# Performance work log

Hardware: AMD Instinct MI355X
Metric: run time of the kernel (lower is better)

Reference implementation:

```python
import jax, jax.numpy as jnp
import numpy as np

B, NN, K, F = 256, 90, 10, 90  # graphs, nodes/graph, retain_node, node_len
TENDENCY = 0.7


def setup_inputs() -> dict:
    key = jax.random.key(0)
    ks = jax.random.split(key, 16)
    N = B * NN
    # fully-connected (no self-loop) edge list per graph, block-offset per graph
    a = np.repeat(np.arange(NN), NN)
    b = np.tile(np.arange(NN), NN)
    m = a != b
    src0, dst0 = a[m], b[m]                      # [8010]
    off = (np.arange(B) * NN)[:, None]
    src = (src0[None, :] + off).ravel()
    dst = (dst0[None, :] + off).ravel()
    edge_index = jnp.asarray(np.stack([src, dst]), dtype=jnp.int64)
    E = edge_index.shape[1]
    batch = jnp.asarray(np.repeat(np.arange(B), NN), dtype=jnp.int64)
    s = 1.0 / np.sqrt(F)
    return {
        "x": jax.random.normal(ks[0], (N, F), jnp.float32),
        "edge_index": edge_index,
        "edge_attr": jax.random.uniform(ks[1], (E,), jnp.float32),
        "batch": batch,
        "W1r": jax.random.normal(ks[2], (F, F), jnp.float32) * s,
        "W1m": jax.random.normal(ks[3], (F, F), jnp.float32) * s,
        "b1": jnp.zeros((F,), jnp.float32),
        "W2r": jax.random.normal(ks[4], (F, F), jnp.float32) * s,
        "W2m": jax.random.normal(ks[5], (F, F), jnp.float32) * s,
        "b2": jnp.zeros((F,), jnp.float32),
        "pool_p": jax.random.normal(ks[6], (F,), jnp.float32),
        "lin_W": jax.random.normal(ks[7], (K * F, 2 * K * F + 1), jnp.float32) / np.sqrt(K * F),
        "lin_b": jnp.zeros((2 * K * F + 1,), jnp.float32),
        "cls_W": jax.random.normal(ks[8], (2 * K * F + 1, 1), jnp.float32) / np.sqrt(2 * K * F + 1),
        "cls_b": jnp.zeros((1,), jnp.float32),
    }


def reference(x, edge_index, edge_attr, batch, W1r, W1m, b1, W2r, W2m, b2,
              pool_p, lin_W, lin_b, cls_W, cls_b):
    src, dst = edge_index[0], edge_index[1]
    N = x.shape[0]

    def conv(h, Wr, Wm, b):  # edge-conditioned message passing
        msg = (h[src] @ Wm) * edge_attr[:, None]          # [E, F]
        agg = jax.ops.segment_sum(msg, dst, num_segments=N)
        return jax.nn.relu(h @ Wr + agg + b)

    def bn(h):  # fresh BatchNorm1d (gamma=1, beta=0), training-mode batch stats
        mu = h.mean(axis=0)
        var = h.var(axis=0)
        return (h - mu) * jax.lax.rsqrt(var + 1e-5)

    x = bn(conv(x, W1r, W1m, b1))
    x = bn(conv(x, W2r, W2m, b2))

    # category-aware top-k pooling: projection score, keep K nodes per graph
    score = TENDENCY * jnp.tanh((x @ pool_p) / jnp.linalg.norm(pool_p))  # [N]
    vals, idx = jax.lax.top_k(score.reshape(B, NN), K)                   # [B, K]
    xb = x.reshape(B, NN, F)
    xs = jnp.take_along_axis(xb, idx[:, :, None], axis=1) * vals[:, :, None]
    perm = (idx + (jnp.arange(B) * NN)[:, None]).reshape(-1)             # global node ids

    h = xs.reshape(B, K * F)
    h = h @ lin_W + lin_b
    out = jax.nn.sigmoid((h @ cls_W + cls_b).reshape(-1))                # [B]
    return (out, perm)
```

## Files before the change

kernel.cpp:

```cpp
#include <hip/hip_runtime.h>
#include <math.h>

#define NG   90
#define PD   96
#define STRD 100
#define KK   10
#define NB   256
#define NTOT (NB*NG)
#define EPG  8010
#define SM_FLOATS (4*PD*STRD + 4*96)

__global__ __launch_bounds__(256)
void prep_v_kernel(const float* __restrict__ linW, const float* __restrict__ linb,
                   const float* __restrict__ clsW, const float* __restrict__ clsb,
                   const float* __restrict__ poolp,
                   float* __restrict__ vlin, float* __restrict__ scal) {
    int b = blockIdx.x, tid = threadIdx.x;
    int lane = tid & 63, w = tid >> 6;
    if (b < 225) {
        int j = b * 4 + w;
        const float* row = linW + (size_t)j * 1801;
        float acc = 0.f;
        for (int c = lane; c < 1801; c += 64) acc += row[c] * clsW[c];
        for (int off = 32; off; off >>= 1) acc += __shfl_down(acc, off);
        if (lane == 0) vlin[j] = acc;
    } else {
        if (w == 0) {
            float acc = 0.f;
            for (int c = lane; c < 1801; c += 64) acc += linb[c] * clsW[c];
            for (int off = 32; off; off >>= 1) acc += __shfl_down(acc, off);
            if (lane == 0) scal[0] = acc + clsb[0];
        } else if (w == 1) {
            float acc = 0.f;
            for (int c = lane; c < NG; c += 64) acc += poolp[c] * poolp[c];
            for (int off = 32; off; off >>= 1) acc += __shfl_down(acc, off);
            if (lane == 0) scal[1] = rsqrtf(acc);
        }
    }
}

__global__ __launch_bounds__(1024, 4)
void layer_kernel(const float* __restrict__ xin, const float* __restrict__ gsIn, int apply_bn,
                  const float* __restrict__ attr,
                  const float* __restrict__ Wm, const float* __restrict__ Wr,
                  const float* __restrict__ bias,
                  float* __restrict__ hout, float* __restrict__ gsOut)
{
    extern __shared__ float sm[];
    float* sX   = sm;
    float* sA   = sX + PD * STRD;
    float* sM   = sA + PD * STRD;
    float* sW   = sM + PD * STRD;
    float* sSum = sW + PD * STRD;
    float* sSq  = sSum + 96;
    float* sMu  = sSq + 96;
    float* sRs  = sMu + 96;

    const int g = blockIdx.x, tid = threadIdx.x;
    const int lane = tid & 63, wave = tid >> 6;
    const int wr = wave >> 2, wc = wave & 3;
    const int lr = lane >> 3, lc = lane & 7;
    const int r0 = (wr * 8 + lr) * 3, c0 = (wc * 8 + lc) * 3;

    if (tid < 96) {
        sSum[tid] = 0.f; sSq[tid] = 0.f;
        float m = 0.f, r = 1.f;
        if (apply_bn && tid < NG) {
            m = gsIn[tid] * (1.f / NTOT);
            float v = gsIn[96 + tid] * (1.f / NTOT) - m * m;
            r = rsqrtf(v + 1e-5f);
        }
        sMu[tid] = m; sRs[tid] = r;
    }
    __syncthreads();

    for (int idx = tid; idx < PD * PD; idx += 1024) {
        int r = idx / PD, k = idx - (idx / PD) * PD;
        float v = 0.f;
        if (r < NG && k < NG) v = (xin[(g * NG + r) * NG + k] - sMu[k]) * sRs[k];
        sX[r * STRD + k] = v;
    }
    for (int idx = tid; idx < PD * PD; idx += 1024) {
        int s = idx / PD, d = idx - (idx / PD) * PD;
        float v = 0.f;
        if (s < NG && d < NG && d != s) v = attr[g * EPG + s * 89 + (d > s ? d - 1 : d)];
        sA[d * STRD + s] = v;
    }
    for (int idx = tid; idx < PD * PD; idx += 1024) {
        int k = idx / PD, c = idx - (idx / PD) * PD;
        float v = (k < NG && c < NG) ? Wm[k * NG + c] : 0.f;
        sW[c * STRD + k] = v;
    }
    float wrg[9];
#pragma unroll
    for (int t = 0; t < 9; t++) {
        int idx = tid + t * 1024;
        int k = idx / PD, c = idx - (idx / PD) * PD;
        wrg[t] = (k < NG && c < NG) ? Wr[k * NG + c] : 0.f;
    }
    float bj[3];
#pragma unroll
    for (int j = 0; j < 3; j++) bj[j] = (c0 + j < NG) ? bias[c0 + j] : 0.f;
    __syncthreads();

    float accM[3][3] = {{0.f,0.f,0.f},{0.f,0.f,0.f},{0.f,0.f,0.f}};
    {
        const float* pX = sX + r0 * STRD;
        const float* pW = sW + c0 * STRD;
#pragma unroll 3
        for (int k = 0; k < PD; k += 4) {
            float4 xv[3], wv[3];
#pragma unroll
            for (int i = 0; i < 3; i++) xv[i] = *(const float4*)(pX + i * STRD + k);
#pragma unroll
            for (int j = 0; j < 3; j++) wv[j] = *(const float4*)(pW + j * STRD + k);
#pragma unroll
            for (int i = 0; i < 3; i++)
#pragma unroll
                for (int j = 0; j < 3; j++) {
                    accM[i][j] = fmaf(xv[i].x, wv[j].x, accM[i][j]);
                    accM[i][j] = fmaf(xv[i].y, wv[j].y, accM[i][j]);
                    accM[i][j] = fmaf(xv[i].z, wv[j].z, accM[i][j]);
                    accM[i][j] = fmaf(xv[i].w, wv[j].w, accM[i][j]);
                }
        }
    }
#pragma unroll
    for (int j = 0; j < 3; j++)
#pragma unroll
        for (int i = 0; i < 3; i++)
            sM[(c0 + j) * STRD + (r0 + i)] = accM[i][j];
    __syncthreads();

#pragma unroll
    for (int t = 0; t < 9; t++) {
        int idx = tid + t * 1024;
        int k = idx / PD, c = idx - (idx / PD) * PD;
        sW[c * STRD + k] = wrg[t];
    }
    __syncthreads();

    float h[3][3];
#pragma unroll
    for (int j = 0; j < 3; j++)
#pragma unroll
        for (int i = 0; i < 3; i++) h[i][j] = bj[j];
    {
        const float* pX = sX + r0 * STRD;
        const float* pA = sA + r0 * STRD;
        const float* pW = sW + c0 * STRD;
        const float* pM = sM + c0 * STRD;
#pragma unroll 2
        for (int k = 0; k < PD; k += 4) {
            float4 xv[3], av[3], wv[3], mv[3];
#pragma unroll
            for (int i = 0; i < 3; i++) {
                xv[i] = *(const float4*)(pX + i * STRD + k);
                av[i] = *(const float4*)(pA + i * STRD + k);
            }
#pragma unroll
            for (int j = 0; j < 3; j++) {
                wv[j] = *(const float4*)(pW + j * STRD + k);
                mv[j] = *(const float4*)(pM + j * STRD + k);
            }
#pragma unroll
            for (int i = 0; i < 3; i++)
#pragma unroll
                for (int j = 0; j < 3; j++) {
                    h[i][j] = fmaf(xv[i].x, wv[j].x, h[i][j]);
                    h[i][j] = fmaf(xv[i].y, wv[j].y, h[i][j]);
                    h[i][j] = fmaf(xv[i].z, wv[j].z, h[i][j]);
                    h[i][j] = fmaf(xv[i].w, wv[j].w, h[i][j]);
                    h[i][j] = fmaf(av[i].x, mv[j].x, h[i][j]);
                    h[i][j] = fmaf(av[i].y, mv[j].y, h[i][j]);
                    h[i][j] = fmaf(av[i].z, mv[j].z, h[i][j]);
                    h[i][j] = fmaf(av[i].w, mv[j].w, h[i][j]);
                }
        }
    }

    float cs[3] = {0.f,0.f,0.f}, cq[3] = {0.f,0.f,0.f};
#pragma unroll
    for (int i = 0; i < 3; i++) {
        int r = r0 + i;
        if (r < NG) {
#pragma unroll
            for (int j = 0; j < 3; j++) {
                int c = c0 + j;
                float v = fmaxf(h[i][j], 0.f);
                if (c < NG) {
                    hout[(size_t)(g * NG + r) * NG + c] = v;
                    cs[j] += v; cq[j] += v * v;
                }
            }
        }
    }
#pragma unroll
    for (int m = 8; m < 64; m <<= 1) {
#pragma unroll
        for (int j = 0; j < 3; j++) {
            cs[j] += __shfl_xor(cs[j], m);
            cq[j] += __shfl_xor(cq[j], m);
        }
    }
    if (lr == 0) {
#pragma unroll
        for (int j = 0; j < 3; j++) {
            int c = c0 + j;
            if (c < NG) { atomicAdd(&sSum[c], cs[j]); atomicAdd(&sSq[c], cq[j]); }
        }
    }
    __syncthreads();
    if (tid < NG) { atomicAdd(&gsOut[tid], sSum[tid]); atomicAdd(&gsOut[96 + tid], sSq[tid]); }
}

__global__ __launch_bounds__(256)
void final_kernel(const float* __restrict__ h2,
                  const float* __restrict__ gsum, const float* __restrict__ gsq,
                  const float* __restrict__ poolp,
                  const float* __restrict__ vlin, const float* __restrict__ scal,
                  float* __restrict__ out)
{
    __shared__ float sXN[NG * 91];
    __shared__ float sMu[96], sRs[96], sP[96];
    __shared__ float sScore[NG];
    __shared__ int   sIdx[KK];
    __shared__ float sVal[KK];
    __shared__ float sRed[4];
    const int g = blockIdx.x, tid = threadIdx.x;

    if (tid < NG) {
        float m = gsum[tid] * (1.f / NTOT);
        float v = gsq[tid] * (1.f / NTOT) - m * m;
        sMu[tid] = m; sRs[tid] = rsqrtf(v + 1e-5f);
        sP[tid] = poolp[tid];
    }
    __syncthreads();

    const float* hg = h2 + (size_t)g * (NG * NG);
    for (int idx = tid; idx < NG * NG; idx += 256) {
        int d = idx / NG, f = idx - (idx / NG) * NG;
        sXN[d * 91 + f] = (hg[idx] - sMu[f]) * sRs[f];
    }
    __syncthreads();

    if (tid < NG) {
        float s = 0.f;
        for (int f = 0; f < NG; f++) s += sXN[tid * 91 + f] * sP[f];
        sScore[tid] = 0.7f * tanhf(s * scal[1]);
    }
    __syncthreads();

    if (tid < 64) {
        float va = sScore[tid];
        float vb = (tid + 64 < NG) ? sScore[tid + 64] : -1e30f;
        int ia = tid, ib = tid + 64;
        for (int k = 0; k < KK; k++) {
            float v; int i;
            if (va >= vb) { v = va; i = ia; } else { v = vb; i = ib; }
            for (int off = 1; off < 64; off <<= 1) {
                float v2 = __shfl_xor(v, off);
                int   i2 = __shfl_xor(i, off);
                if (v2 > v || (v2 == v && i2 < i)) { v = v2; i = i2; }
            }
            if (tid == 0) { sIdx[k] = i; sVal[k] = v; }
            if (i == ia) va = -1e30f;
            if (i == ib) vb = -1e30f;
        }
    }
    __syncthreads();

    if (tid < KK) out[NB + g * KK + tid] = (float)(g * NG + sIdx[tid]);

    float acc = 0.f;
    for (int j = tid; j < KK * NG; j += 256) {
        int k = j / NG, f = j - (j / NG) * NG;
        acc += sXN[sIdx[k] * 91 + f] * sVal[k] * vlin[j];
    }
    for (int off = 32; off; off >>= 1) acc += __shfl_down(acc, off);
    if ((tid & 63) == 0) sRed[tid >> 6] = acc;
    __syncthreads();
    if (tid == 0) {
        float tot = sRed[0] + sRed[1] + sRed[2] + sRed[3] + scal[0];
        out[g] = 1.f / (1.f + expf(-tot));
    }
}

extern "C" void kernel_launch(void* const* d_in, const int* in_sizes, int n_in,
                              void* d_out, int out_size, void* d_ws, size_t ws_size,
                              hipStream_t stream) {
    const float* x    = (const float*)d_in[0];
    const float* attr = (const float*)d_in[2];
    const float* W1r  = (const float*)d_in[4];
    const float* W1m  = (const float*)d_in[5];
    const float* b1   = (const float*)d_in[6];
    const float* W2r  = (const float*)d_in[7];
    const float* W2m  = (const float*)d_in[8];
    const float* b2   = (const float*)d_in[9];
    const float* poolp= (const float*)d_in[10];
    const float* linW = (const float*)d_in[11];
    const float* linb = (const float*)d_in[12];
    const float* clsW = (const float*)d_in[13];
    const float* clsb = (const float*)d_in[14];

    float* ws     = (float*)d_ws;
    float* gstats = ws;
    float* vlin   = ws + 384;
    float* scal   = ws + 1284;
    float* h1     = ws + 2048;
    float* h2     = h1 + (size_t)NTOT * NG;

    hipMemsetAsync(gstats, 0, 384 * sizeof(float), stream);
    prep_v_kernel<<<226, 256, 0, stream>>>(linW, linb, clsW, clsb, poolp, vlin, scal);

    const size_t smem = SM_FLOATS * sizeof(float);
    layer_kernel<<<NB, 1024, smem, stream>>>(x,  gstats, 0, attr, W1m, W1r, b1, h1, gstats);
    layer_kernel<<<NB, 1024, smem, stream>>>(h1, gstats, 1, attr, W2m, W2r, b2, h2, gstats + 192);

    final_kernel<<<NB, 256, 0, stream>>>(h2, gstats + 192, gstats + 288, poolp, vlin, scal, (float*)d_out);
}
```

Measured before the change: 197.1 us.

## Use 6x6 register tiles with 256 threads and fuse prep into layer kernel

Result: slower. 241.7 us (+22.6%).

```diff
diff --git a/kernel.cpp b/kernel.cpp
--- a/kernel.cpp
+++ b/kernel.cpp
@@ -8,59 +8,36 @@
 #define NB   256
 #define NTOT (NB*NG)
 #define EPG  8010
-#define SM_FLOATS (4*PD*STRD + 4*96)
-
-__global__ __launch_bounds__(256)
-void prep_v_kernel(const float* __restrict__ linW, const float* __restrict__ linb,
-                   const float* __restrict__ clsW, const float* __restrict__ clsb,
-                   const float* __restrict__ poolp,
-                   float* __restrict__ vlin, float* __restrict__ scal) {
-    int b = blockIdx.x, tid = threadIdx.x;
-    int lane = tid & 63, w = tid >> 6;
-    if (b < 225) {
-        int j = b * 4 + w;
-        const float* row = linW + (size_t)j * 1801;
-        float acc = 0.f;
-        for (int c = lane; c < 1801; c += 64) acc += row[c] * clsW[c];
-        for (int off = 32; off; off >>= 1) acc += __shfl_down(acc, off);
-        if (lane == 0) vlin[j] = acc;
-    } else {
-        if (w == 0) {
-            float acc = 0.f;
-            for (int c = lane; c < 1801; c += 64) acc += linb[c] * clsW[c];
-            for (int off = 32; off; off >>= 1) acc += __shfl_down(acc, off);
-            if (lane == 0) scal[0] = acc + clsb[0];
-        } else if (w == 1) {
-            float acc = 0.f;
-            for (int c = lane; c < NG; c += 64) acc += poolp[c] * poolp[c];
-            for (int off = 32; off; off >>= 1) acc += __shfl_down(acc, off);
-            if (lane == 0) scal[1] = rsqrtf(acc);
-        }
-    }
-}
-
-__global__ __launch_bounds__(1024, 4)
+#define ARR  (PD*STRD)
+#define SM_FLOATS (4*ARR + 4*96)
+
+__global__ __launch_bounds__(256, 1)
 void layer_kernel(const float* __restrict__ xin, const float* __restrict__ gsIn, int apply_bn,
                   const float* __restrict__ attr,
                   const float* __restrict__ Wm, const float* __restrict__ Wr,
                   const float* __restrict__ bias,
-                  float* __restrict__ hout, float* __restrict__ gsOut)
+                  float* __restrict__ hout, float* __restrict__ gsOut,
+                  int do_prep,
+                  const float* __restrict__ linW, const float* __restrict__ linb,
+                  const float* __restrict__ clsW, const float* __restrict__ clsb,
+                  const float* __restrict__ poolp,
+                  float* __restrict__ vlin, float* __restrict__ scal)
 {
     extern __shared__ float sm[];
-    float* sX   = sm;
-    float* sA   = sX + PD * STRD;
-    float* sM   = sA + PD * STRD;
-    float* sW   = sM + PD * STRD;
-    float* sSum = sW + PD * STRD;
+    float* sXM = sm;
+    float* sA  = sXM + ARR;
+    float* sWm = sA + ARR;
+    float* sWr = sWm + ARR;
+    float* sSum = sWr + ARR;
     float* sSq  = sSum + 96;
     float* sMu  = sSq + 96;
     float* sRs  = sMu + 96;
 
     const int g = blockIdx.x, tid = threadIdx.x;
     const int lane = tid & 63, wave = tid >> 6;
-    const int wr = wave >> 2, wc = wave & 3;
     const int lr = lane >> 3, lc = lane & 7;
-    const int r0 = (wr * 8 + lr) * 3, c0 = (wc * 8 + lc) * 3;
+    const int r0 = (wave >> 1) * 48 + lr * 6;
+    const int c0 = (wave & 1) * 48 + lc * 6;
 
     if (tid < 96) {
         sSum[tid] = 0.f; sSq[tid] = 0.f;
@@ -74,103 +51,92 @@
     }
     __syncthreads();
 
-    for (int idx = tid; idx < PD * PD; idx += 1024) {
+    for (int idx = tid; idx < PD * PD; idx += 256) {
         int r = idx / PD, k = idx - (idx / PD) * PD;
         float v = 0.f;
-        if (r < NG && k < NG) v = (xin[(g * NG + r) * NG + k] - sMu[k]) * sRs[k];
-        sX[r * STRD + k] = v;
-    }
-    for (int idx = tid; idx < PD * PD; idx += 1024) {
-        int s = idx / PD, d = idx - (idx / PD) * PD;
+        if (r < NG && k < NG) v = (xin[(size_t)(g * NG + r) * NG + k] - sMu[k]) * sRs[k];
+        sXM[r * STRD + k] = v;
+    }
+    for (int idx = tid; idx < PD * PD; idx += 256) {
+        int d = idx / PD, s = idx - (idx / PD) * PD;
         float v = 0.f;
-        if (s < NG && d < NG && d != s) v = attr[g * EPG + s * 89 + (d > s ? d - 1 : d)];
+        if (d < NG && s < NG && s != d) v = attr[(size_t)g * EPG + s * 89 + (d > s ? d - 1 : d)];
         sA[d * STRD + s] = v;
     }
-    for (int idx = tid; idx < PD * PD; idx += 1024) {
-        int k = idx / PD, c = idx - (idx / PD) * PD;
-        float v = (k < NG && c < NG) ? Wm[k * NG + c] : 0.f;
-        sW[c * STRD + k] = v;
-    }
-    float wrg[9];
-#pragma unroll
-    for (int t = 0; t < 9; t++) {
-        int idx = tid + t * 1024;
-        int k = idx / PD, c = idx - (idx / PD) * PD;
-        wrg[t] = (k < NG && c < NG) ? Wr[k * NG + c] : 0.f;
-    }
-    float bj[3];
-#pragma unroll
-    for (int j = 0; j < 3; j++) bj[j] = (c0 + j < NG) ? bias[c0 + j] : 0.f;
-    __syncthreads();
-
-    float accM[3][3] = {{0.f,0.f,0.f},{0.f,0.f,0.f},{0.f,0.f,0.f}};
+    for (int idx = tid; idx < PD * PD; idx += 256) {
+        int c = idx / PD, k = idx - (idx / PD) * PD;
+        float vm = 0.f, vr = 0.f;
+        if (c < NG && k < NG) { vm = Wm[k * NG + c]; vr = Wr[k * NG + c]; }
+        sWm[c * STRD + k] = vm;
+        sWr[c * STRD + k] = vr;
+    }
+    float bj[6];
+#pragma unroll
+    for (int j = 0; j < 6; j++) bj[j] = (c0 + j < NG) ? bias[c0 + j] : 0.f;
+    __syncthreads();
+
+    float accM[6][6], accR[6][6];
+#pragma unroll
+    for (int i = 0; i < 6; i++)
+#pragma unroll
+        for (int j = 0; j < 6; j++) { accM[i][j] = 0.f; accR[i][j] = 0.f; }
     {
-        const float* pX = sX + r0 * STRD;
-        const float* pW = sW + c0 * STRD;
-#pragma unroll 3
-        for (int k = 0; k < PD; k += 4) {
-            float4 xv[3], wv[3];
-#pragma unroll
-            for (int i = 0; i < 3; i++) xv[i] = *(const float4*)(pX + i * STRD + k);
-#pragma unroll
-            for (int j = 0; j < 3; j++) wv[j] = *(const float4*)(pW + j * STRD + k);
-#pragma unroll
-            for (int i = 0; i < 3; i++)
-#pragma unroll
-                for (int j = 0; j < 3; j++) {
-                    accM[i][j] = fmaf(xv[i].x, wv[j].x, accM[i][j]);
-                    accM[i][j] = fmaf(xv[i].y, wv[j].y, accM[i][j]);
-                    accM[i][j] = fmaf(xv[i].z, wv[j].z, accM[i][j]);
-                    accM[i][j] = fmaf(xv[i].w, wv[j].w, accM[i][j]);
-                }
-        }
-    }
-#pragma unroll
-    for (int j = 0; j < 3; j++)
-#pragma unroll
-        for (int i = 0; i < 3; i++)
-            sM[(c0 + j) * STRD + (r0 + i)] = accM[i][j];
-    __syncthreads();
-
-#pragma unroll
-    for (int t = 0; t < 9; t++) {
-        int idx = tid + t * 1024;
-        int k = idx / PD, c = idx - (idx / PD) * PD;
-        sW[c * STRD + k] = wrg[t];
-    }
-    __syncthreads();
-
-    float h[3][3];
-#pragma unroll
-    for (int j = 0; j < 3; j++)
-#pragma unroll
-        for (int i = 0; i < 3; i++) h[i][j] = bj[j];
-    {
-        const float* pX = sX + r0 * STRD;
-        const float* pA = sA + r0 * STRD;
-        const float* pW = sW + c0 * STRD;
-        const float* pM = sM + c0 * STRD;
+        const float* pX  = sXM + r0 * STRD;
+        const float* pWm = sWm + c0 * STRD;
+        const float* pWr = sWr + c0 * STRD;
 #pragma unroll 2
         for (int k = 0; k < PD; k += 4) {
-            float4 xv[3], av[3], wv[3], mv[3];
-#pragma unroll
-            for (int i = 0; i < 3; i++) {
-                xv[i] = *(const float4*)(pX + i * STRD + k);
-                av[i] = *(const float4*)(pA + i * STRD + k);
+            float4 xv[6], wm[6], wr[6];
+#pragma unroll
+            for (int i = 0; i < 6; i++) xv[i] = *(const float4*)(pX + i * STRD + k);
+#pragma unroll
+            for (int j = 0; j < 6; j++) {
+                wm[j] = *(const float4*)(pWm + j * STRD + k);
+                wr[j] = *(const float4*)(pWr + j * STRD + k);
             }
 #pragma unroll
-            for (int j = 0; j < 3; j++) {
-                wv[j] = *(const float4*)(pW + j * STRD + k);
-                mv[j] = *(const float4*)(pM + j * STRD + k);
-            }
-#pragma unroll
-            for (int i = 0; i < 3; i++)
-#pragma unroll
-                for (int j = 0; j < 3; j++) {
-                    h[i][j] = fmaf(xv[i].x, wv[j].x, h[i][j]);
-                    h[i][j] = fmaf(xv[i].y, wv[j].y, h[i][j]);
-                    h[i][j] = fmaf(xv[i].z, wv[j].z, h[i][j]);
-                    h[i][j] = fmaf(xv[i].w, wv[j].w, h[i][j]);
+            for (int i = 0; i < 6; i++)
+#pragma unroll
+                for (int j = 0; j < 6; j++) {
+                    accM[i][j] = fmaf(xv[i].x, wm[j].x, accM[i][j]);
+                    accM[i][j] = fmaf(xv[i].y, wm[j].y, accM[i][j]);
+                    accM[i][j] = fmaf(xv[i].z, wm[j].z, accM[i][j]);
+                    accM[i][j] = fmaf(xv[i].w, wm[j].w, accM[i][j]);
+                    accR[i][j] = fmaf(xv[i].x, wr[j].x, accR[i][j]);
+                    accR[i][j] = fmaf(xv[i].y, wr[j].y, accR[i][j]);
+                    accR[i][j] = fmaf(xv[i].z, wr[j].z, accR[i][j]);
+                    accR[i][j] = fmaf(xv[i].w, wr[j].w, accR[i][j]);
+                }
+        }
+    }
+    __syncthreads();
+
+#pragma unroll
+    for (int j = 0; j < 6; j++)
+#pragma unroll
+        for (int i = 0; i < 6; i++)
+            sXM[(c0 + j) * STRD + (r0 + i)] = accM[i][j];
+    __syncthreads();
+
+    float h[6][6];
+#pragma unroll
+    for (int i = 0; i < 6; i++)
+#pragma unroll
+        for (int j = 0; j < 6; j++) h[i][j] = accR[i][j] + bj[j];
+    {
+        const float* pA = sA  + r0 * STRD;
+        const float* pM = sXM + c0 * STRD;
+#pragma unroll 2
+        for (int k = 0; k < PD; k += 4) {
+            float4 av[6], mv[6];
+#pragma unroll
+            for (int i = 0; i < 6; i++) av[i] = *(const float4*)(pA + i * STRD + k);
+#pragma unroll
+            for (int j = 0; j < 6; j++) mv[j] = *(const float4*)(pM + j * STRD + k);
+#pragma unroll
+            for (int i = 0; i < 6; i++)
+#pragma unroll
+                for (int j = 0; j < 6; j++) {
                     h[i][j] = fmaf(av[i].x, mv[j].x, h[i][j]);
                     h[i][j] = fmaf(av[i].y, mv[j].y, h[i][j]);
                     h[i][j] = fmaf(av[i].z, mv[j].z, h[i][j]);
@@ -179,16 +145,18 @@
         }
     }
 
-    float cs[3] = {0.f,0.f,0.f}, cq[3] = {0.f,0.f,0.f};
-#pragma unroll
-    for (int i = 0; i < 3; i++) {
+    float cs[6], cq[6];
+#pragma unroll
+    for (int j = 0; j < 6; j++) { cs[j] = 0.f; cq[j] = 0.f; }
+#pragma unroll
+    for (int i = 0; i < 6; i++) {
         int r = r0 + i;
         if (r < NG) {
 #pragma unroll
-            for (int j = 0; j < 3; j++) {
+            for (int j = 0; j < 6; j++) {
                 int c = c0 + j;
-                float v = fmaxf(h[i][j], 0.f);
                 if (c < NG) {
+                    float v = fmaxf(h[i][j], 0.f);
                     hout[(size_t)(g * NG + r) * NG + c] = v;
                     cs[j] += v; cq[j] += v * v;
                 }
@@ -198,20 +166,43 @@
 #pragma unroll
     for (int m = 8; m < 64; m <<= 1) {
 #pragma unroll
-        for (int j = 0; j < 3; j++) {
+        for (int j = 0; j < 6; j++) {
             cs[j] += __shfl_xor(cs[j], m);
             cq[j] += __shfl_xor(cq[j], m);
         }
     }
     if (lr == 0) {
 #pragma unroll
-        for (int j = 0; j < 3; j++) {
+        for (int j = 0; j < 6; j++) {
             int c = c0 + j;
             if (c < NG) { atomicAdd(&sSum[c], cs[j]); atomicAdd(&sSq[c], cq[j]); }
         }
     }
     __syncthreads();
     if (tid < NG) { atomicAdd(&gsOut[tid], sSum[tid]); atomicAdd(&gsOut[96 + tid], sSq[tid]); }
+
+    if (do_prep) {
+        if (g < 225) {
+            int j = g * 4 + wave;
+            const float* row = linW + (size_t)j * 1801;
+            float acc = 0.f;
+            for (int c = lane; c < 1801; c += 64) acc += row[c] * clsW[c];
+            for (int off = 32; off; off >>= 1) acc += __shfl_down(acc, off);
+            if (lane == 0) vlin[j] = acc;
+        } else if (g == 255) {
+            if (wave == 0) {
+                float acc = 0.f;
+                for (int c = lane; c < 1801; c += 64) acc += linb[c] * clsW[c];
+                for (int off = 32; off; off >>= 1) acc += __shfl_down(acc, off);
+                if (lane == 0) scal[0] = acc + clsb[0];
+            } else if (wave == 1) {
+                float acc = 0.f;
+                for (int c = lane; c < NG; c += 64) acc += poolp[c] * poolp[c];
+                for (int off = 32; off; off >>= 1) acc += __shfl_down(acc, off);
+                if (lane == 0) scal[1] = rsqrtf(acc);
+            }
+        }
+    }
 }
 
 __global__ __launch_bounds__(256)
@@ -311,11 +302,14 @@
     float* h2     = h1 + (size_t)NTOT * NG;
 
     hipMemsetAsync(gstats, 0, 384 * sizeof(float), stream);
-    prep_v_kernel<<<226, 256, 0, stream>>>(linW, linb, clsW, clsb, poolp, vlin, scal);
 
     const size_t smem = SM_FLOATS * sizeof(float);
-    layer_kernel<<<NB, 1024, smem, stream>>>(x,  gstats, 0, attr, W1m, W1r, b1, h1, gstats);
-    layer_kernel<<<NB, 1024, smem, stream>>>(h1, gstats, 1, attr, W2m, W2r, b2, h2, gstats + 192);
+    hipFuncSetAttribute((const void*)layer_kernel, hipFuncAttributeMaxDynamicSharedMemorySize, (int)smem);
+
+    layer_kernel<<<NB, 256, smem, stream>>>(x,  gstats, 0, attr, W1m, W1r, b1, h1, gstats,
+                                            1, linW, linb, clsW, clsb, poolp, vlin, scal);
+    layer_kernel<<<NB, 256, smem, stream>>>(h1, gstats, 1, attr, W2m, W2r, b2, h2, gstats + 192,
+                                            0, linW, linb, clsW, clsb, poolp, vlin, scal);
 
     final_kernel<<<NB, 256, 0, stream>>>(h2, gstats + 192, gstats + 288, poolp, vlin, scal, (float*)d_out);
 }
```

## Fuse all stages into one persistent kernel with grid-wide atomic barriers

Applied to the files above, without the earlier changes.

Result: slower. 464.0 us (+135.4%).

```diff
diff --git a/kernel.cpp b/kernel.cpp
--- a/kernel.cpp
+++ b/kernel.cpp
@@ -4,250 +4,234 @@
 #define NG   90
 #define PD   96
 #define STRD 100
+#define ARR  (PD*STRD)
 #define KK   10
 #define NB   256
 #define NTOT (NB*NG)
 #define EPG  8010
-#define SM_FLOATS (4*PD*STRD + 4*96)
-
-__global__ __launch_bounds__(256)
-void prep_v_kernel(const float* __restrict__ linW, const float* __restrict__ linb,
-                   const float* __restrict__ clsW, const float* __restrict__ clsb,
-                   const float* __restrict__ poolp,
-                   float* __restrict__ vlin, float* __restrict__ scal) {
-    int b = blockIdx.x, tid = threadIdx.x;
-    int lane = tid & 63, w = tid >> 6;
-    if (b < 225) {
-        int j = b * 4 + w;
-        const float* row = linW + (size_t)j * 1801;
-        float acc = 0.f;
-        for (int c = lane; c < 1801; c += 64) acc += row[c] * clsW[c];
-        for (int off = 32; off; off >>= 1) acc += __shfl_down(acc, off);
-        if (lane == 0) vlin[j] = acc;
-    } else {
-        if (w == 0) {
-            float acc = 0.f;
-            for (int c = lane; c < 1801; c += 64) acc += linb[c] * clsW[c];
-            for (int off = 32; off; off >>= 1) acc += __shfl_down(acc, off);
-            if (lane == 0) scal[0] = acc + clsb[0];
-        } else if (w == 1) {
-            float acc = 0.f;
-            for (int c = lane; c < NG; c += 64) acc += poolp[c] * poolp[c];
-            for (int off = 32; off; off >>= 1) acc += __shfl_down(acc, off);
-            if (lane == 0) scal[1] = rsqrtf(acc);
-        }
-    }
+#define SM_FLOATS (4*ARR)
+
+__device__ __forceinline__ float agent_loadf(const float* p) {
+    return __hip_atomic_load(p, __ATOMIC_RELAXED, __HIP_MEMORY_SCOPE_AGENT);
 }
 
 __global__ __launch_bounds__(1024, 4)
-void layer_kernel(const float* __restrict__ xin, const float* __restrict__ gsIn, int apply_bn,
-                  const float* __restrict__ attr,
-                  const float* __restrict__ Wm, const float* __restrict__ Wr,
-                  const float* __restrict__ bias,
-                  float* __restrict__ hout, float* __restrict__ gsOut)
+void mega_kernel(const float* __restrict__ x, const float* __restrict__ attr,
+                 const float* __restrict__ W1m, const float* __restrict__ W1r, const float* __restrict__ b1,
+                 const float* __restrict__ W2m, const float* __restrict__ W2r, const float* __restrict__ b2,
+                 const float* __restrict__ poolp, const float* __restrict__ linW, const float* __restrict__ linb,
+                 const float* __restrict__ clsW, const float* __restrict__ clsb,
+                 float* __restrict__ gstats, float* __restrict__ vlin, float* __restrict__ scal,
+                 unsigned int* __restrict__ bar, float* __restrict__ out)
 {
     extern __shared__ float sm[];
-    float* sX   = sm;
-    float* sA   = sX + PD * STRD;
-    float* sM   = sA + PD * STRD;
-    float* sW   = sM + PD * STRD;
-    float* sSum = sW + PD * STRD;
-    float* sSq  = sSum + 96;
-    float* sMu  = sSq + 96;
-    float* sRs  = sMu + 96;
+    float* s0  = sm;
+    float* sA  = s0 + ARR;
+    float* sWm = sA + ARR;
+    float* sWr = sWm + ARR;
+    __shared__ float sSum[96], sSq[96];
+    __shared__ float sScore[96], sP[96];
+    __shared__ float sVal[KK];
+    __shared__ int   sIdx[KK];
+    __shared__ float sRed[16];
 
     const int g = blockIdx.x, tid = threadIdx.x;
     const int lane = tid & 63, wave = tid >> 6;
-    const int wr = wave >> 2, wc = wave & 3;
-    const int lr = lane >> 3, lc = lane & 7;
-    const int r0 = (wr * 8 + lr) * 3, c0 = (wc * 8 + lc) * 3;
-
-    if (tid < 96) {
-        sSum[tid] = 0.f; sSq[tid] = 0.f;
-        float m = 0.f, r = 1.f;
-        if (apply_bn && tid < NG) {
-            m = gsIn[tid] * (1.f / NTOT);
-            float v = gsIn[96 + tid] * (1.f / NTOT) - m * m;
-            r = rsqrtf(v + 1e-5f);
-        }
-        sMu[tid] = m; sRs[tid] = r;
-    }
-    __syncthreads();
+    const int lr = (lane >> 3) & 7, lc = lane & 7;
+    const int r0 = ((wave >> 2) * 8 + lr) * 3;
+    const int c0 = ((wave & 3) * 8 + lc) * 3;
+
+    if (tid < 96) { sSum[tid] = 0.f; sSq[tid] = 0.f; }
+    if (tid < NG) sP[tid] = poolp[tid];
 
     for (int idx = tid; idx < PD * PD; idx += 1024) {
         int r = idx / PD, k = idx - (idx / PD) * PD;
-        float v = 0.f;
-        if (r < NG && k < NG) v = (xin[(g * NG + r) * NG + k] - sMu[k]) * sRs[k];
-        sX[r * STRD + k] = v;
+        s0[r * STRD + k] = (r < NG && k < NG) ? x[(size_t)(g * NG + r) * NG + k] : 0.f;
     }
     for (int idx = tid; idx < PD * PD; idx += 1024) {
         int s = idx / PD, d = idx - (idx / PD) * PD;
         float v = 0.f;
-        if (s < NG && d < NG && d != s) v = attr[g * EPG + s * 89 + (d > s ? d - 1 : d)];
+        if (s < NG && d < NG && d != s) v = attr[(size_t)g * EPG + s * 89 + (d > s ? d - 1 : d)];
         sA[d * STRD + s] = v;
     }
     for (int idx = tid; idx < PD * PD; idx += 1024) {
         int k = idx / PD, c = idx - (idx / PD) * PD;
-        float v = (k < NG && c < NG) ? Wm[k * NG + c] : 0.f;
-        sW[c * STRD + k] = v;
-    }
-    float wrg[9];
-#pragma unroll
-    for (int t = 0; t < 9; t++) {
-        int idx = tid + t * 1024;
-        int k = idx / PD, c = idx - (idx / PD) * PD;
-        wrg[t] = (k < NG && c < NG) ? Wr[k * NG + c] : 0.f;
-    }
-    float bj[3];
-#pragma unroll
-    for (int j = 0; j < 3; j++) bj[j] = (c0 + j < NG) ? bias[c0 + j] : 0.f;
+        bool ok = (k < NG && c < NG);
+        sWm[c * STRD + k] = ok ? W1m[k * NG + c] : 0.f;
+        sWr[c * STRD + k] = ok ? W1r[k * NG + c] : 0.f;
+    }
     __syncthreads();
 
-    float accM[3][3] = {{0.f,0.f,0.f},{0.f,0.f,0.f},{0.f,0.f,0.f}};
-    {
-        const float* pX = sX + r0 * STRD;
-        const float* pW = sW + c0 * STRD;
-#pragma unroll 3
-        for (int k = 0; k < PD; k += 4) {
-            float4 xv[3], wv[3];
-#pragma unroll
-            for (int i = 0; i < 3; i++) xv[i] = *(const float4*)(pX + i * STRD + k);
-#pragma unroll
-            for (int j = 0; j < 3; j++) wv[j] = *(const float4*)(pW + j * STRD + k);
+    float h[3][3];
+
+    for (int layer = 0; layer < 2; ++layer) {
+        float accM[3][3] = {{0.f,0.f,0.f},{0.f,0.f,0.f},{0.f,0.f,0.f}};
+        float accR[3][3] = {{0.f,0.f,0.f},{0.f,0.f,0.f},{0.f,0.f,0.f}};
+        {
+            const float* pX = s0  + r0 * STRD;
+            const float* pm = sWm + c0 * STRD;
+            const float* pr = sWr + c0 * STRD;
+#pragma unroll 2
+            for (int k = 0; k < PD; k += 4) {
+                float4 xv[3], wm[3], wr[3];
+#pragma unroll
+                for (int i = 0; i < 3; i++) xv[i] = *(const float4*)(pX + i * STRD + k);
+#pragma unroll
+                for (int j = 0; j < 3; j++) {
+                    wm[j] = *(const float4*)(pm + j * STRD + k);
+                    wr[j] = *(const float4*)(pr + j * STRD + k);
+                }
+#pragma unroll
+                for (int i = 0; i < 3; i++)
+#pragma unroll
+                    for (int j = 0; j < 3; j++) {
+                        accM[i][j] = fmaf(xv[i].x, wm[j].x, accM[i][j]);
+                        accM[i][j] = fmaf(xv[i].y, wm[j].y, accM[i][j]);
+                        accM[i][j] = fmaf(xv[i].z, wm[j].z, accM[i][j]);
+                        accM[i][j] = fmaf(xv[i].w, wm[j].w, accM[i][j]);
+                        accR[i][j] = fmaf(xv[i].x, wr[j].x, accR[i][j]);
+                        accR[i][j] = fmaf(xv[i].y, wr[j].y, accR[i][j]);
+                        accR[i][j] = fmaf(xv[i].z, wr[j].z, accR[i][j]);
+                        accR[i][j] = fmaf(xv[i].w, wr[j].w, accR[i][j]);
+                    }
+            }
+        }
+        __syncthreads();
+#pragma unroll
+        for (int j = 0; j < 3; j++)
 #pragma unroll
             for (int i = 0; i < 3; i++)
-#pragma unroll
-                for (int j = 0; j < 3; j++) {
-                    accM[i][j] = fmaf(xv[i].x, wv[j].x, accM[i][j]);
-                    accM[i][j] = fmaf(xv[i].y, wv[j].y, accM[i][j]);
-                    accM[i][j] = fmaf(xv[i].z, wv[j].z, accM[i][j]);
-                    accM[i][j] = fmaf(xv[i].w, wv[j].w, accM[i][j]);
-                }
-        }
-    }
-#pragma unroll
-    for (int j = 0; j < 3; j++)
-#pragma unroll
-        for (int i = 0; i < 3; i++)
-            sM[(c0 + j) * STRD + (r0 + i)] = accM[i][j];
-    __syncthreads();
-
-#pragma unroll
-    for (int t = 0; t < 9; t++) {
-        int idx = tid + t * 1024;
-        int k = idx / PD, c = idx - (idx / PD) * PD;
-        sW[c * STRD + k] = wrg[t];
-    }
-    __syncthreads();
-
-    float h[3][3];
-#pragma unroll
-    for (int j = 0; j < 3; j++)
-#pragma unroll
-        for (int i = 0; i < 3; i++) h[i][j] = bj[j];
-    {
-        const float* pX = sX + r0 * STRD;
-        const float* pA = sA + r0 * STRD;
-        const float* pW = sW + c0 * STRD;
-        const float* pM = sM + c0 * STRD;
+                s0[(c0 + j) * STRD + (r0 + i)] = accM[i][j];
+        __syncthreads();
+
+        const float* bias = layer ? b2 : b1;
+#pragma unroll
+        for (int j = 0; j < 3; j++) {
+            float bj = (c0 + j < NG) ? bias[c0 + j] : 0.f;
+#pragma unroll
+            for (int i = 0; i < 3; i++) h[i][j] = accR[i][j] + bj;
+        }
+        {
+            const float* pA = sA + r0 * STRD;
+            const float* pM = s0 + c0 * STRD;
 #pragma unroll 2
-        for (int k = 0; k < PD; k += 4) {
-            float4 xv[3], av[3], wv[3], mv[3];
-#pragma unroll
-            for (int i = 0; i < 3; i++) {
-                xv[i] = *(const float4*)(pX + i * STRD + k);
-                av[i] = *(const float4*)(pA + i * STRD + k);
-            }
+            for (int k = 0; k < PD; k += 4) {
+                float4 av[3], mv[3];
+#pragma unroll
+                for (int i = 0; i < 3; i++) av[i] = *(const float4*)(pA + i * STRD + k);
+#pragma unroll
+                for (int j = 0; j < 3; j++) mv[j] = *(const float4*)(pM + j * STRD + k);
+#pragma unroll
+                for (int i = 0; i < 3; i++)
+#pragma unroll
+                    for (int j = 0; j < 3; j++) {
+                        h[i][j] = fmaf(av[i].x, mv[j].x, h[i][j]);
+                        h[i][j] = fmaf(av[i].y, mv[j].y, h[i][j]);
+                        h[i][j] = fmaf(av[i].z, mv[j].z, h[i][j]);
+                        h[i][j] = fmaf(av[i].w, mv[j].w, h[i][j]);
+                    }
+            }
+        }
+
+        float cs[3] = {0.f,0.f,0.f}, cq[3] = {0.f,0.f,0.f};
+#pragma unroll
+        for (int i = 0; i < 3; i++) {
+            int r = r0 + i;
 #pragma unroll
             for (int j = 0; j < 3; j++) {
-                wv[j] = *(const float4*)(pW + j * STRD + k);
-                mv[j] = *(const float4*)(pM + j * STRD + k);
-            }
-#pragma unroll
-            for (int i = 0; i < 3; i++)
-#pragma unroll
-                for (int j = 0; j < 3; j++) {
-                    h[i][j] = fmaf(xv[i].x, wv[j].x, h[i][j]);
-                    h[i][j] = fmaf(xv[i].y, wv[j].y, h[i][j]);
-                    h[i][j] = fmaf(xv[i].z, wv[j].z, h[i][j]);
-                    h[i][j] = fmaf(xv[i].w, wv[j].w, h[i][j]);
-                    h[i][j] = fmaf(av[i].x, mv[j].x, h[i][j]);
-                    h[i][j] = fmaf(av[i].y, mv[j].y, h[i][j]);
-                    h[i][j] = fmaf(av[i].z, mv[j].z, h[i][j]);
-                    h[i][j] = fmaf(av[i].w, mv[j].w, h[i][j]);
-                }
-        }
-    }
-
-    float cs[3] = {0.f,0.f,0.f}, cq[3] = {0.f,0.f,0.f};
-#pragma unroll
-    for (int i = 0; i < 3; i++) {
-        int r = r0 + i;
-        if (r < NG) {
+                float v = fmaxf(h[i][j], 0.f);
+                h[i][j] = v;
+                if (r < NG && c0 + j < NG) { cs[j] += v; cq[j] += v * v; }
+            }
+        }
+#pragma unroll
+        for (int m = 8; m < 64; m <<= 1) {
+#pragma unroll
+            for (int j = 0; j < 3; j++) {
+                cs[j] += __shfl_xor(cs[j], m);
+                cq[j] += __shfl_xor(cq[j], m);
+            }
+        }
+        if (lr == 0) {
 #pragma unroll
             for (int j = 0; j < 3; j++) {
                 int c = c0 + j;
-                float v = fmaxf(h[i][j], 0.f);
-                if (c < NG) {
-                    hout[(size_t)(g * NG + r) * NG + c] = v;
-                    cs[j] += v; cq[j] += v * v;
+                if (c < NG) { atomicAdd(&sSum[c], cs[j]); atomicAdd(&sSq[c], cq[j]); }
+            }
+        }
+        __syncthreads();
+        float* gs = gstats + layer * 192;
+        if (tid < NG) { atomicAdd(&gs[tid], sSum[tid]); atomicAdd(&gs[96 + tid], sSq[tid]); }
+        __syncthreads();
+
+        if (tid == 0)
+            __hip_atomic_fetch_add(&bar[layer], 1u, __ATOMIC_RELEASE, __HIP_MEMORY_SCOPE_AGENT);
+        if (layer == 0) {
+            if (g < 225) {
+                if (wave < 4) {
+                    int row = g * 4 + wave;
+                    const float* rw = linW + (size_t)row * 1801;
+                    float acc = 0.f;
+                    for (int c2 = lane; c2 < 1801; c2 += 64) acc += rw[c2] * clsW[c2];
+                    for (int off = 32; off; off >>= 1) acc += __shfl_down(acc, off);
+                    if (lane == 0) vlin[row] = acc;
                 }
-            }
-        }
-    }
-#pragma unroll
-    for (int m = 8; m < 64; m <<= 1) {
-#pragma unroll
-        for (int j = 0; j < 3; j++) {
-            cs[j] += __shfl_xor(cs[j], m);
-            cq[j] += __shfl_xor(cq[j], m);
-        }
-    }
-    if (lr == 0) {
+            } else if (g == 255) {
+                if (wave == 0) {
+                    float acc = 0.f;
+                    for (int c2 = lane; c2 < 1801; c2 += 64) acc += linb[c2] * clsW[c2];
+                    for (int off = 32; off; off >>= 1) acc += __shfl_down(acc, off);
+                    if (lane == 0) scal[0] = acc + clsb[0];
+                } else if (wave == 1) {
+                    float acc = 0.f;
+                    for (int c2 = lane; c2 < NG; c2 += 64) acc += poolp[c2] * poolp[c2];
+                    for (int off = 32; off; off >>= 1) acc += __shfl_down(acc, off);
+                    if (lane == 0) scal[1] = rsqrtf(acc);
+                }
+            }
+        }
+        if (tid == 0) {
+            int it = 0;
+            while (__hip_atomic_load(&bar[layer], __ATOMIC_ACQUIRE, __HIP_MEMORY_SCOPE_AGENT) < (unsigned)NB) {
+                __builtin_amdgcn_s_sleep(4);
+                if (++it > 300000) break;
+            }
+        }
+        __syncthreads();
+
+        float mu[3], rs[3];
 #pragma unroll
         for (int j = 0; j < 3; j++) {
             int c = c0 + j;
-            if (c < NG) { atomicAdd(&sSum[c], cs[j]); atomicAdd(&sSq[c], cq[j]); }
-        }
-    }
-    __syncthreads();
-    if (tid < NG) { atomicAdd(&gsOut[tid], sSum[tid]); atomicAdd(&gsOut[96 + tid], sSq[tid]); }
-}
-
-__global__ __launch_bounds__(256)
-void final_kernel(const float* __restrict__ h2,
-                  const float* __restrict__ gsum, const float* __restrict__ gsq,
-                  const float* __restrict__ poolp,
-                  const float* __restrict__ vlin, const float* __restrict__ scal,
-                  float* __restrict__ out)
-{
-    __shared__ float sXN[NG * 91];
-    __shared__ float sMu[96], sRs[96], sP[96];
-    __shared__ float sScore[NG];
-    __shared__ int   sIdx[KK];
-    __shared__ float sVal[KK];
-    __shared__ float sRed[4];
-    const int g = blockIdx.x, tid = threadIdx.x;
-
-    if (tid < NG) {
-        float m = gsum[tid] * (1.f / NTOT);
-        float v = gsq[tid] * (1.f / NTOT) - m * m;
-        sMu[tid] = m; sRs[tid] = rsqrtf(v + 1e-5f);
-        sP[tid] = poolp[tid];
-    }
-    __syncthreads();
-
-    const float* hg = h2 + (size_t)g * (NG * NG);
-    for (int idx = tid; idx < NG * NG; idx += 256) {
-        int d = idx / NG, f = idx - (idx / NG) * NG;
-        sXN[d * 91 + f] = (hg[idx] - sMu[f]) * sRs[f];
-    }
-    __syncthreads();
-
+            float s1 = agent_loadf(gs + c), s2 = agent_loadf(gs + 96 + c);
+            float m = s1 * (1.f / NTOT);
+            float v = s2 * (1.f / NTOT) - m * m;
+            mu[j] = m; rs[j] = rsqrtf(v + 1e-5f);
+        }
+#pragma unroll
+        for (int i = 0; i < 3; i++)
+#pragma unroll
+            for (int j = 0; j < 3; j++) {
+                float v = (h[i][j] - mu[j]) * rs[j];
+                s0[(r0 + i) * STRD + (c0 + j)] = (r0 + i < NG && c0 + j < NG) ? v : 0.f;
+            }
+        if (layer == 0) {
+            if (tid < 96) { sSum[tid] = 0.f; sSq[tid] = 0.f; }
+            for (int idx = tid; idx < PD * PD; idx += 1024) {
+                int k = idx / PD, c = idx - (idx / PD) * PD;
+                bool ok = (k < NG && c < NG);
+                sWm[c * STRD + k] = ok ? W2m[k * NG + c] : 0.f;
+                sWr[c * STRD + k] = ok ? W2r[k * NG + c] : 0.f;
+            }
+        }
+        __syncthreads();
+    }
+
+    float sc1 = agent_loadf(scal + 1);
     if (tid < NG) {
         float s = 0.f;
-        for (int f = 0; f < NG; f++) s += sXN[tid * 91 + f] * sP[f];
-        sScore[tid] = 0.7f * tanhf(s * scal[1]);
+        for (int f = 0; f < NG; f++) s += s0[tid * STRD + f] * sP[f];
+        sScore[tid] = 0.7f * tanhf(s * sc1);
     }
     __syncthreads();
 
@@ -273,15 +257,17 @@
     if (tid < KK) out[NB + g * KK + tid] = (float)(g * NG + sIdx[tid]);
 
     float acc = 0.f;
-    for (int j = tid; j < KK * NG; j += 256) {
-        int k = j / NG, f = j - (j / NG) * NG;
-        acc += sXN[sIdx[k] * 91 + f] * sVal[k] * vlin[j];
+    if (tid < KK * NG) {
+        int k = tid / NG, f = tid - (tid / NG) * NG;
+        acc = s0[sIdx[k] * STRD + f] * sVal[k] * agent_loadf(vlin + tid);
     }
     for (int off = 32; off; off >>= 1) acc += __shfl_down(acc, off);
-    if ((tid & 63) == 0) sRed[tid >> 6] = acc;
+    if (lane == 0) sRed[wave] = acc;
     __syncthreads();
     if (tid == 0) {
-        float tot = sRed[0] + sRed[1] + sRed[2] + sRed[3] + scal[0];
+        float tot = agent_loadf(scal);
+#pragma unroll
+        for (int w = 0; w < 16; w++) tot += sRed[w];
         out[g] = 1.f / (1.f + expf(-tot));
     }
 }
@@ -303,19 +289,19 @@
     const float* clsW = (const float*)d_in[13];
     const float* clsb = (const float*)d_in[14];
 
-    float* ws     = (float*)d_ws;
-    float* gstats = ws;
-    float* vlin   = ws + 384;
-    float* scal   = ws + 1284;
-    float* h1     = ws + 2048;
-    float* h2     = h1 + (size_t)NTOT * NG;
-
-    hipMemsetAsync(gstats, 0, 384 * sizeof(float), stream);
-    prep_v_kernel<<<226, 256, 0, stream>>>(linW, linb, clsW, clsb, poolp, vlin, scal);
+    float* ws       = (float*)d_ws;
+    float* gstats   = ws;
+    unsigned int* bar = (unsigned int*)(ws + 384);
+    float* vlin     = ws + 392;
+    float* scal     = ws + 1292;
+    float* out      = (float*)d_out;
+
+    hipMemsetAsync(ws, 0, 392 * sizeof(float), stream);
 
     const size_t smem = SM_FLOATS * sizeof(float);
-    layer_kernel<<<NB, 1024, smem, stream>>>(x,  gstats, 0, attr, W1m, W1r, b1, h1, gstats);
-    layer_kernel<<<NB, 1024, smem, stream>>>(h1, gstats, 1, attr, W2m, W2r, b2, h2, gstats + 192);
-
-    final_kernel<<<NB, 256, 0, stream>>>(h2, gstats + 192, gstats + 288, poolp, vlin, scal, (float*)d_out);
+    hipFuncSetAttribute((const void*)mega_kernel, hipFuncAttributeMaxDynamicSharedMemorySize, (int)smem);
+
+    mega_kernel<<<NB, 1024, smem, stream>>>(x, attr, W1m, W1r, b1, W2m, W2r, b2,
+                                            poolp, linW, linb, clsW, clsb,
+                                            gstats, vlin, scal, bar, out);
 }
```
